# Kernel optimization log

Hardware: AMD Instinct MI355X
Metric: run time of the kernel (lower is better)

Reference implementation:

```python
import jax, jax.numpy as jnp
import numpy as np
import itertools

GROUP_DIM = 3
N_GROUPS = 256          # total_dim // group_dim = 768 // 3
TEMP = 0.3

# base hypercube {-1,+1}^3 -> [8, 3], fixed buffer
BASE_CODEBOOK = jnp.asarray(
    list(itertools.product([-1.0, 1.0], repeat=GROUP_DIM)), dtype=jnp.float32)


def setup_inputs() -> dict:
    key = jax.random.key(0)
    k1, k2 = jax.random.split(key)
    x = jax.random.normal(k1, (8, 4096, 768), dtype=jnp.float32)
    delta = jax.random.normal(k2, (8, 3), dtype=jnp.float32) * 0.1
    deform_scale = jnp.asarray(0.05, dtype=jnp.float32)
    return {"x": x, "delta": delta, "deform_scale": deform_scale}


def reference(x, delta, deform_scale):
    B, S, D = x.shape
    cb = BASE_CODEBOOK + deform_scale * delta            # [K=8, g=3]
    groups = x.reshape(B, S, N_GROUPS, GROUP_DIM)        # [B,S,G,g]
    cb_norm_sq = jnp.sum(cb * cb, axis=1)                # [K]
    z_norm_sq = jnp.sum(groups * groups, axis=-1, keepdims=True)  # [B,S,G,1]
    cross = jnp.einsum('bsgd,kd->bsgk', groups, cb)      # [B,S,G,K]
    dists_sq = z_norm_sq - 2.0 * cross + cb_norm_sq      # [B,S,G,K]
    weights = jax.nn.softmax(-dists_sq / TEMP, axis=-1)  # [B,S,G,K]
    quantized = jnp.einsum('bsgk,kd->bsgd', weights, cb).reshape(B, S, D)
    # straight-through estimator
    return x + jax.lax.stop_gradient(quantized - x)
```

## Files before the change

kernel.cpp:

```cpp
#include <hip/hip_runtime.h>


#define TEMP_INV (1.0f / 0.3f)

__global__ __launch_bounds__(256) void dq_kernel(
    const float* __restrict__ x,
    const float* __restrict__ delta,
    const float* __restrict__ scale_p,
    float* __restrict__ out,
    int nchunks)
{
    const int idx = blockIdx.x * blockDim.x + threadIdx.x;

    const float s = *scale_p;
    float cb[8][3];
    float w[8][3];
    float b[8];
    #pragma unroll
    for (int k = 0; k < 8; ++k) {
        #pragma unroll
        for (int d = 0; d < 3; ++d) {
            const float base = ((k >> (2 - d)) & 1) ? 1.0f : -1.0f;
            const float c = fmaf(s, delta[k * 3 + d], base);
            cb[k][d] = c;
            w[k][d] = 2.0f * TEMP_INV * c;
        }
        b[k] = -(cb[k][0] * cb[k][0] + cb[k][1] * cb[k][1] + cb[k][2] * cb[k][2]) * TEMP_INV;
    }

    if (idx >= nchunks) return;

    const float4* xin = reinterpret_cast<const float4*>(x) + (size_t)idx * 3;
    const float4 v0 = xin[0], v1 = xin[1], v2 = xin[2];
    float zin[12] = {v0.x, v0.y, v0.z, v0.w,
                     v1.x, v1.y, v1.z, v1.w,
                     v2.x, v2.y, v2.z, v2.w};
    float zo[12];

    #pragma unroll
    for (int g = 0; g < 4; ++g) {
        const float z0 = zin[g * 3 + 0];
        const float z1 = zin[g * 3 + 1];
        const float z2 = zin[g * 3 + 2];

        float logit[8];
        float m = -1e30f;
        #pragma unroll
        for (int k = 0; k < 8; ++k) {
            const float l = fmaf(z0, w[k][0], fmaf(z1, w[k][1], fmaf(z2, w[k][2], b[k])));
            logit[k] = l;
            m = fmaxf(m, l);
        }

        float e[8];
        float sum = 0.0f;
        #pragma unroll
        for (int k = 0; k < 8; ++k) {
            e[k] = __expf(logit[k] - m);
            sum += e[k];
        }
        const float inv = 1.0f / sum;

        float q0 = 0.0f, q1 = 0.0f, q2 = 0.0f;
        #pragma unroll
        for (int k = 0; k < 8; ++k) {
            q0 = fmaf(e[k], cb[k][0], q0);
            q1 = fmaf(e[k], cb[k][1], q1);
            q2 = fmaf(e[k], cb[k][2], q2);
        }
        zo[g * 3 + 0] = q0 * inv;
        zo[g * 3 + 1] = q1 * inv;
        zo[g * 3 + 2] = q2 * inv;
    }

    float4* o = reinterpret_cast<float4*>(out) + (size_t)idx * 3;
    o[0] = make_float4(zo[0], zo[1], zo[2], zo[3]);
    o[1] = make_float4(zo[4], zo[5], zo[6], zo[7]);
    o[2] = make_float4(zo[8], zo[9], zo[10], zo[11]);
}

extern "C" void kernel_launch(void* const* d_in, const int* in_sizes, int n_in,
                              void* d_out, int out_size, void* d_ws, size_t ws_size,
                              hipStream_t stream) {
    const float* x     = (const float*)d_in[0];
    const float* delta = (const float*)d_in[1];
    const float* scale = (const float*)d_in[2];
    float* out = (float*)d_out;

    const int total = out_size;
    const int nchunks = total / 12;
    const int block = 256;
    const int grid = (nchunks + block - 1) / block;

    dq_kernel<<<grid, block, 0, stream>>>(x, delta, scale, out, nchunks);
}
```

Baseline: 39.30 us.

## Stage tiles through LDS for coalesced loads and use exp2/rcp intrinsics

Each block now loads its 3072-float tile with fully coalesced float4 accesses, stages it in shared memory, and reads each thread's 12-element chunk back from LDS. Outputs are written to LDS and stored with coalesced float4 stores. The softmax folds the ln2 factor into the weights so it can use the hardware exp2 and fast reciprocal, and it reuses the scaled weights for the weighted sum. The bounds check is removed, so the launch assumes the size is a multiple of 3072, and the kernel adds two barriers plus LDS traffic.

```diff
diff --git a/kernel.cpp b/kernel.cpp
--- a/kernel.cpp
+++ b/kernel.cpp
@@ -1,40 +1,53 @@
 #include <hip/hip_runtime.h>
 
 
-#define TEMP_INV (1.0f / 0.3f)
+#define TEMP 0.3f
+#define LN2  0.6931471805599453f
 
 __global__ __launch_bounds__(256) void dq_kernel(
     const float* __restrict__ x,
     const float* __restrict__ delta,
     const float* __restrict__ scale_p,
-    float* __restrict__ out,
-    int nchunks)
+    float* __restrict__ out)
 {
-    const int idx = blockIdx.x * blockDim.x + threadIdx.x;
+    __shared__ float4 lin[768];
+    __shared__ float4 lout[768];
+
+    const int t = threadIdx.x;
+    const size_t base4 = (size_t)blockIdx.x * 768;
+
+    const float4* xin = reinterpret_cast<const float4*>(x) + base4;
+    const float4 g0 = xin[t];
+    const float4 g1 = xin[t + 256];
+    const float4 g2 = xin[t + 512];
 
     const float s = *scale_p;
-    float cb[8][3];
-    float w[8][3];
-    float b[8];
+    const float c1 = 2.0f / (TEMP * LN2);
+    const float c2 = 1.0f / (TEMP * LN2);
+    const float K  = TEMP * LN2 * 0.5f;
+    float w0[8], w1[8], w2[8], b[8];
     #pragma unroll
     for (int k = 0; k < 8; ++k) {
-        #pragma unroll
-        for (int d = 0; d < 3; ++d) {
-            const float base = ((k >> (2 - d)) & 1) ? 1.0f : -1.0f;
-            const float c = fmaf(s, delta[k * 3 + d], base);
-            cb[k][d] = c;
-            w[k][d] = 2.0f * TEMP_INV * c;
-        }
-        b[k] = -(cb[k][0] * cb[k][0] + cb[k][1] * cb[k][1] + cb[k][2] * cb[k][2]) * TEMP_INV;
+        const float d0 = fmaf(s, delta[k * 3 + 0], (k & 4) ? 1.0f : -1.0f);
+        const float d1 = fmaf(s, delta[k * 3 + 1], (k & 2) ? 1.0f : -1.0f);
+        const float d2 = fmaf(s, delta[k * 3 + 2], (k & 1) ? 1.0f : -1.0f);
+        w0[k] = c1 * d0;
+        w1[k] = c1 * d1;
+        w2[k] = c1 * d2;
+        b[k]  = -(d0 * d0 + d1 * d1 + d2 * d2) * c2;
     }
 
-    if (idx >= nchunks) return;
+    lin[t]       = g0;
+    lin[t + 256] = g1;
+    lin[t + 512] = g2;
+    __syncthreads();
 
-    const float4* xin = reinterpret_cast<const float4*>(x) + (size_t)idx * 3;
-    const float4 v0 = xin[0], v1 = xin[1], v2 = xin[2];
-    float zin[12] = {v0.x, v0.y, v0.z, v0.w,
-                     v1.x, v1.y, v1.z, v1.w,
-                     v2.x, v2.y, v2.z, v2.w};
+    const float4 a0 = lin[3 * t + 0];
+    const float4 a1 = lin[3 * t + 1];
+    const float4 a2 = lin[3 * t + 2];
+    const float zin[12] = {a0.x, a0.y, a0.z, a0.w,
+                           a1.x, a1.y, a1.z, a1.w,
+                           a2.x, a2.y, a2.z, a2.w};
     float zo[12];
 
     #pragma unroll
@@ -47,7 +60,7 @@
         float m = -1e30f;
         #pragma unroll
         for (int k = 0; k < 8; ++k) {
-            const float l = fmaf(z0, w[k][0], fmaf(z1, w[k][1], fmaf(z2, w[k][2], b[k])));
+            const float l = fmaf(z0, w0[k], fmaf(z1, w1[k], fmaf(z2, w2[k], b[k])));
             logit[k] = l;
             m = fmaxf(m, l);
         }
@@ -56,27 +69,32 @@
         float sum = 0.0f;
         #pragma unroll
         for (int k = 0; k < 8; ++k) {
-            e[k] = __expf(logit[k] - m);
+            e[k] = __builtin_amdgcn_exp2f(logit[k] - m);
             sum += e[k];
         }
-        const float inv = 1.0f / sum;
+        const float inv = K * __builtin_amdgcn_rcpf(sum);
 
         float q0 = 0.0f, q1 = 0.0f, q2 = 0.0f;
         #pragma unroll
         for (int k = 0; k < 8; ++k) {
-            q0 = fmaf(e[k], cb[k][0], q0);
-            q1 = fmaf(e[k], cb[k][1], q1);
-            q2 = fmaf(e[k], cb[k][2], q2);
+            q0 = fmaf(e[k], w0[k], q0);
+            q1 = fmaf(e[k], w1[k], q1);
+            q2 = fmaf(e[k], w2[k], q2);
         }
         zo[g * 3 + 0] = q0 * inv;
         zo[g * 3 + 1] = q1 * inv;
         zo[g * 3 + 2] = q2 * inv;
     }
 
-    float4* o = reinterpret_cast<float4*>(out) + (size_t)idx * 3;
-    o[0] = make_float4(zo[0], zo[1], zo[2], zo[3]);
-    o[1] = make_float4(zo[4], zo[5], zo[6], zo[7]);
-    o[2] = make_float4(zo[8], zo[9], zo[10], zo[11]);
+    lout[3 * t + 0] = make_float4(zo[0], zo[1],  zo[2],  zo[3]);
+    lout[3 * t + 1] = make_float4(zo[4], zo[5],  zo[6],  zo[7]);
+    lout[3 * t + 2] = make_float4(zo[8], zo[9],  zo[10], zo[11]);
+    __syncthreads();
+
+    float4* o = reinterpret_cast<float4*>(out) + base4;
+    o[t]       = lout[t];
+    o[t + 256] = lout[t + 256];
+    o[t + 512] = lout[t + 512];
 }
 
 extern "C" void kernel_launch(void* const* d_in, const int* in_sizes, int n_in,
@@ -87,10 +105,6 @@
     const float* scale = (const float*)d_in[2];
     float* out = (float*)d_out;
 
-    const int total = out_size;
-    const int nchunks = total / 12;
-    const int block = 256;
-    const int grid = (nchunks + block - 1) / block;
-
-    dq_kernel<<<grid, block, 0, stream>>>(x, delta, scale, out, nchunks);
+    const int grid = out_size / 3072;
+    dq_kernel<<<grid, 256, 0, stream>>>(x, delta, scale, out);
 }
```

New measurement: 35.15 us. 10.6% less time.
